# Optimization experiments

Measured on AMD Instinct MI355X. Metric: run time of the kernel, lower is better.

Reference implementation:

```python
import jax, jax.numpy as jnp
import numpy as np

B, D, H, E, L = 8192, 1024, 1024, 16, 2  # batch, input_dim, exp_hidden_dim, exp_num, exp_layers


def setup_inputs() -> dict:
    key = jax.random.key(0)
    ks = jax.random.split(key, 12)
    s_in = 1.0 / np.sqrt(D)
    s_h = 1.0 / np.sqrt(H)
    return {
        "x":   jax.random.normal(ks[0], (B, D), dtype=jnp.float32),
        # per-expert embedding layer (E experts fused on leading axis)
        "W1":  jax.random.uniform(ks[1], (E, D, H), jnp.float32, -s_in, s_in),
        "b1":  jax.random.uniform(ks[2], (E, H), jnp.float32, -s_in, s_in),
        # per-expert hidden layer (shared across the L repeated blocks, as in the torch code)
        "W2":  jax.random.uniform(ks[3], (E, H, H), jnp.float32, -s_h, s_h),
        "b2":  jax.random.uniform(ks[4], (E, H), jnp.float32, -s_h, s_h),
        # per-expert output layer H -> 1
        "Wo":  jax.random.uniform(ks[5], (E, H), jnp.float32, -s_h, s_h),
        "bo":  jax.random.uniform(ks[6], (E,), jnp.float32, -s_h, s_h),
        # two gates: D -> E, softmax
        "Wg1": jax.random.uniform(ks[7], (D, E), jnp.float32, -s_in, s_in),
        "bg1": jax.random.uniform(ks[8], (E,), jnp.float32, -s_in, s_in),
        "Wg2": jax.random.uniform(ks[9], (D, E), jnp.float32, -s_in, s_in),
        "bg2": jax.random.uniform(ks[10], (E,), jnp.float32, -s_in, s_in),
    }


def reference(x, W1, b1, W2, b2, Wo, bo, Wg1, bg1, Wg2, bg2):
    # Batched experts: h [B, E, H]
    h = jax.nn.sigmoid(jnp.einsum("bd,edh->beh", x, W1) + b1)
    for _ in range(L):  # weight-shared hidden blocks (ReLU then the SAME linear)
        h = jnp.einsum("beh,ehk->bek", jax.nn.relu(h), W2) + b2
    f = jnp.einsum("beh,eh->be", h, Wo) + bo  # expert scalar outputs [B, E]
    g1 = jax.nn.softmax(x @ Wg1 + bg1, axis=-1)  # [B, E]
    g2 = jax.nn.softmax(x @ Wg2 + bg2, axis=-1)
    out1 = jnp.einsum("be,be->b", g1, f)
    out2 = jnp.einsum("be,be->b", g2, f)
    return (out1, out2)
```

## Files before the change

### kernel.cpp

```cpp
#include <hip/hip_runtime.h>
#include <hip/hip_bf16.h>
#include <cstdint>
#include <cstddef>


using half8   = __attribute__((ext_vector_type(8))) _Float16;
using floatx4 = __attribute__((ext_vector_type(4))) float;

template<int ACT>
__global__ __launch_bounds__(256, 2)
void gemm_kernel(const _Float16* __restrict__ A, const _Float16* __restrict__ Bt,
                 const float* __restrict__ bias, _Float16* __restrict__ C,
                 size_t a_estride,
                 const float* __restrict__ Wo, float* __restrict__ f, int e0)
{
    __shared__ __align__(16) _Float16 sbuf[2][24 * 512];

    const int tid  = threadIdx.x;
    const int lane = tid & 63;
    const int w    = tid >> 6;
    const int wm   = w & 1;
    const int wn   = w >> 1;

    const int flat = blockIdx.x + (blockIdx.y << 3);
    const int xcd  = flat & 7;
    int s = flat >> 3;
    const int g = gridDim.y >> 5;
    int le, mb_base;
    if (g <= 8) {
        const int p = 8 / g;
        le = xcd / p;
        mb_base = (xcd % p) * (64 / p);
    } else {
        le = (xcd << 1) | (s >> 8);
        s &= 255;
        mb_base = 0;
    }
    const int nb = (s >> 2) & 3;
    const int mb = mb_base + (s >> 4) * 4 + (s & 3);
    const int m0 = mb * 128;
    const int n0 = nb * 256;

    const _Float16* Ae = A    + (size_t)le * a_estride;
    const _Float16* Be = Bt   + (size_t)le * (1024ull * 1024ull);
    const float*    be = bias + (size_t)le * 1024ull;
    _Float16*       Ce = C    + (size_t)le * (8192ull * 1024ull);

    const int mtb_blk = m0 >> 4;
    const int ntb_blk = n0 >> 4;

    const _Float16* gs[6];
#pragma unroll
    for (int u = 0; u < 6; ++u) {
        const int fidx = w * 6 + u;
        gs[u] = (fidx < 8)
            ? (Ae + (size_t)(mtb_blk + fidx) * (32 * 512) + lane * 8)
            : (Be + (size_t)(ntb_blk + (fidx - 8)) * (32 * 512) + lane * 8);
    }

    floatx4 acc[4][8];
#pragma unroll
    for (int i = 0; i < 4; ++i)
#pragma unroll
        for (int j = 0; j < 8; ++j) { floatx4 z = {0.f, 0.f, 0.f, 0.f}; acc[i][j] = z; }

    auto STAGE = [&](_Float16* buf) {
#pragma unroll
        for (int u = 0; u < 6; ++u) {
            __builtin_amdgcn_global_load_lds(
                (const __attribute__((address_space(1))) void*)gs[u],
                (__attribute__((address_space(3))) void*)(buf + (w * 6 + u) * 512),
                16, 0, 0);
            gs[u] += 512;
        }
    };
    auto COMPUTE = [&](const _Float16* buf) {
        half8 a[4], b[8];
#pragma unroll
        for (int i = 0; i < 4; ++i)
            a[i] = *(const half8*)(buf + (wm * 4 + i) * 512 + lane * 8);
#pragma unroll
        for (int j = 0; j < 8; ++j)
            b[j] = *(const half8*)(buf + 4096 + (wn * 8 + j) * 512 + lane * 8);
#pragma unroll
        for (int i = 0; i < 4; ++i)
#pragma unroll
            for (int j = 0; j < 8; ++j)
                acc[i][j] = __builtin_amdgcn_mfma_f32_16x16x32_f16(a[i], b[j], acc[i][j], 0, 0, 0);
    };

    STAGE(sbuf[0]);
    __syncthreads();
#pragma unroll 1
    for (int c = 0; c < 30; c += 2) {
        STAGE(sbuf[1]);
        COMPUTE(sbuf[0]);
        __syncthreads();
        STAGE(sbuf[0]);
        COMPUTE(sbuf[1]);
        __syncthreads();
    }
    STAGE(sbuf[1]);
    COMPUTE(sbuf[0]);
    __syncthreads();
    COMPUTE(sbuf[1]);

    const int q   = lane >> 4;
    const int l15 = lane & 15;
    float bj[8];
#pragma unroll
    for (int j = 0; j < 8; ++j) bj[j] = be[n0 + wn * 128 + j * 16 + l15];

    if (ACT == 2) {
        const float* we = Wo + (size_t)(e0 + le) * 1024;
        float wj[8];
#pragma unroll
        for (int j = 0; j < 8; ++j) wj[j] = we[n0 + wn * 128 + j * 16 + l15];
#pragma unroll
        for (int i = 0; i < 4; ++i) {
            const int mbase = m0 + wm * 64 + i * 16 + q * 4;
#pragma unroll
            for (int r = 0; r < 4; ++r) {
                float sacc = 0.f;
#pragma unroll
                for (int j = 0; j < 8; ++j)
                    sacc += fmaxf(acc[i][j][r] + bj[j], 0.0f) * wj[j];
#pragma unroll
                for (int m = 1; m < 16; m <<= 1) sacc += __shfl_xor(sacc, m, 64);
                if (l15 == 0) atomicAdd(&f[(size_t)(mbase + r) * 16 + (e0 + le)], sacc);
            }
        }
    } else {
        __syncthreads();
        _Float16* T = &sbuf[0][0] + w * 3072;
        const int kcg0 = (n0 + wn * 128) >> 5;
#pragma unroll
        for (int i = 0; i < 4; ++i) {
#pragma unroll
            for (int j = 0; j < 8; ++j)
#pragma unroll
                for (int r = 0; r < 4; ++r) {
                    float v = acc[i][j][r] + bj[j];
                    v = 1.0f / (1.0f + __expf(-v));
                    T[(q * 4 + r) * 136 + j * 16 + l15] = (_Float16)v;
                }
            const int mt = mtb_blk + wm * 4 + i;
#pragma unroll
            for (int kci = 0; kci < 4; ++kci) {
                half8 v8 = *(const half8*)(T + l15 * 136 + kci * 32 + q * 8);
                *(half8*)(Ce + ((size_t)mt * 32 + kcg0 + kci) * 512 + lane * 8) = v8;
            }
        }
    }
}

__global__ __launch_bounds__(256)
void castx_kernel(const float* __restrict__ x, _Float16* __restrict__ xb)
{
    __shared__ _Float16 tile[64 * 72];
    const int k0 = blockIdx.x * 64;
    const int m0 = blockIdx.y * 64;
    const int tid = threadIdx.x;
    const int col4 = (tid & 15) * 4;
    const int rb   = tid >> 4;
#pragma unroll
    for (int p = 0; p < 4; ++p) {
        const int row = rb + p * 16;
        float4 a = *(const float4*)(x + (size_t)(m0 + row) * 1024 + k0 + col4);
        _Float16* d = tile + row * 72 + col4;
        d[0] = (_Float16)a.x; d[1] = (_Float16)a.y; d[2] = (_Float16)a.z; d[3] = (_Float16)a.w;
    }
    __syncthreads();
    const int lane = tid & 63, w = tid >> 6;
    const int l15 = lane & 15, q = lane >> 4;
#pragma unroll
    for (int ff = 0; ff < 2; ++ff) {
        const int fidx = w * 2 + ff;
        const int mi = fidx >> 1, kci = fidx & 1;
        half8 v = *(const half8*)(tile + (mi * 16 + l15) * 72 + kci * 32 + q * 8);
        const size_t mt = (m0 >> 4) + mi, kc = (k0 >> 5) + kci;
        *(half8*)(xb + (mt * 32 + kc) * 512 + lane * 8) = v;
    }
}

__global__ __launch_bounds__(256)
void wtr_kernel(const float* __restrict__ W1, const float* __restrict__ W2,
                _Float16* __restrict__ W1F, _Float16* __restrict__ W2F,
                const float* __restrict__ Wo, float* __restrict__ v)
{
    __shared__ _Float16 tile[64 * 73];
    const int z = blockIdx.z;
    const float* src = (z < 16) ? (W1 + (size_t)z * 1048576ull) : (W2 + (size_t)(z - 16) * 1048576ull);
    _Float16*    dst = (z < 16) ? (W1F + (size_t)z * 1048576ull) : (W2F + (size_t)(z - 16) * 1048576ull);
    const int n0 = blockIdx.x * 64;
    const int k0 = blockIdx.y * 64;
    const int tid = threadIdx.x;
    const int lane = tid & 63, w = tid >> 6;
    const int l15 = lane & 15, q = lane >> 4;

    const int col4 = l15 * 4;
    const int rbase = w * 4 + q;
    float4 a4[4];
#pragma unroll
    for (int p = 0; p < 4; ++p) {
        const int row = rbase + p * 16;
        a4[p] = *(const float4*)(src + (size_t)(k0 + row) * 1024 + n0 + col4);
        _Float16* d = tile + row * 73 + col4;
        d[0] = (_Float16)a4[p].x; d[1] = (_Float16)a4[p].y;
        d[2] = (_Float16)a4[p].z; d[3] = (_Float16)a4[p].w;
    }

    if (z >= 16) {
        const int e = z - 16;
        const float* wo = Wo + ((size_t)e << 10) + n0;
        float* ve = v + ((size_t)e << 10) + k0;
#pragma unroll
        for (int p = 0; p < 4; ++p) {
            float s = a4[p].x * wo[col4] + a4[p].y * wo[col4 + 1]
                    + a4[p].z * wo[col4 + 2] + a4[p].w * wo[col4 + 3];
            s += __shfl_xor(s, 1, 64);
            s += __shfl_xor(s, 2, 64);
            s += __shfl_xor(s, 4, 64);
            s += __shfl_xor(s, 8, 64);
            if (l15 == 0) atomicAdd(&ve[rbase + p * 16], s);
        }
    }

    __syncthreads();
#pragma unroll
    for (int ff = 0; ff < 2; ++ff) {
        const int fidx = w * 2 + ff;
        const int nti = fidx >> 1, kci = fidx & 1;
        half8 hv;
#pragma unroll
        for (int jj = 0; jj < 8; ++jj)
            hv[jj] = tile[(kci * 32 + q * 8 + jj) * 73 + nti * 16 + l15];
        const size_t nt = (n0 >> 4) + nti, kc = (k0 >> 5) + kci;
        *(half8*)(dst + (nt * 32 + kc) * 512 + lane * 8) = hv;
    }
}

__global__ __launch_bounds__(256)
void zerof_kernel(float* __restrict__ f)
{
    const size_t i = ((size_t)blockIdx.x * 256 + threadIdx.x) * 4;
    float4 z = {0.f, 0.f, 0.f, 0.f};
    *(float4*)(f + i) = z;
}

__global__ __launch_bounds__(64)
void prep_bo2_kernel(const float* __restrict__ b2, const float* __restrict__ Wo,
                     const float* __restrict__ bo, float* __restrict__ bo2)
{
    const int e = blockIdx.x;
    const int lane = threadIdx.x;
    const float* br = b2 + ((size_t)e << 10);
    const float* wo = Wo + ((size_t)e << 10);
    float s = 0.f;
#pragma unroll
    for (int t = 0; t < 16; ++t) s += br[t * 64 + lane] * wo[t * 64 + lane];
#pragma unroll
    for (int m = 1; m < 64; m <<= 1) s += __shfl_xor(s, m, 64);
    if (lane == 0) bo2[e] = s + bo[e];
}

__global__ __launch_bounds__(256)
void final_kernel(const float* __restrict__ x,
                  const float* __restrict__ Wg1, const float* __restrict__ bg1,
                  const float* __restrict__ Wg2, const float* __restrict__ bg2,
                  const float* __restrict__ f, const float* __restrict__ bo2,
                  float* __restrict__ out)
{
    const int lane = threadIdx.x & 63;
    const int w    = threadIdx.x >> 6;
    const int b    = blockIdx.x * 8 + w * 2;
    const float* xA = x + (size_t)b * 1024;
    const float* xB = xA + 1024;
    float g1A[16], g2A[16], g1B[16], g2B[16];
#pragma unroll
    for (int e = 0; e < 16; ++e) { g1A[e] = 0.f; g2A[e] = 0.f; g1B[e] = 0.f; g2B[e] = 0.f; }
#pragma unroll 2
    for (int t = 0; t < 16; ++t) {
        const int d = t * 64 + lane;
        const float xa = xA[d];
        const float xb2 = xB[d];
        const float4* w1 = (const float4*)(Wg1 + (size_t)d * 16);
        const float4* w2 = (const float4*)(Wg2 + (size_t)d * 16);
#pragma unroll
        for (int q4 = 0; q4 < 4; ++q4) {
            const float4 c1 = w1[q4];
            const float4 c2 = w2[q4];
#pragma unroll
            for (int c = 0; c < 4; ++c) {
                const int e = q4 * 4 + c;
                const float v1 = (c == 0) ? c1.x : (c == 1) ? c1.y : (c == 2) ? c1.z : c1.w;
                const float v2 = (c == 0) ? c2.x : (c == 1) ? c2.y : (c == 2) ? c2.z : c2.w;
                g1A[e] += xa * v1; g1B[e] += xb2 * v1;
                g2A[e] += xa * v2; g2B[e] += xb2 * v2;
            }
        }
    }
#pragma unroll
    for (int e = 0; e < 16; ++e) {
#pragma unroll
        for (int m = 1; m < 64; m <<= 1) {
            g1A[e] += __shfl_xor(g1A[e], m, 64);
            g2A[e] += __shfl_xor(g2A[e], m, 64);
            g1B[e] += __shfl_xor(g1B[e], m, 64);
            g2B[e] += __shfl_xor(g2B[e], m, 64);
        }
    }
    const float* fbA = f + (size_t)b * 16;
    const float* fbB = fbA + 16;
#pragma unroll
    for (int rr = 0; rr < 2; ++rr) {
        const float* gp1 = rr ? g1B : g1A;
        const float* gp2 = rr ? g2B : g2A;
        const float* fb  = rr ? fbB : fbA;
        float a1[16], a2[16], m1 = -1e30f, m2 = -1e30f;
#pragma unroll
        for (int e = 0; e < 16; ++e) {
            a1[e] = gp1[e] + bg1[e]; m1 = fmaxf(m1, a1[e]);
            a2[e] = gp2[e] + bg2[e]; m2 = fmaxf(m2, a2[e]);
        }
        float s1 = 0.f, s2 = 0.f, o1 = 0.f, o2 = 0.f;
#pragma unroll
        for (int e = 0; e < 16; ++e) {
            a1[e] = __expf(a1[e] - m1); s1 += a1[e];
            a2[e] = __expf(a2[e] - m2); s2 += a2[e];
        }
#pragma unroll
        for (int e = 0; e < 16; ++e) {
            const float fe = fb[e] + bo2[e];
            o1 += a1[e] * fe; o2 += a2[e] * fe;
        }
        if (lane == 0) { out[b + rr] = o1 / s1; out[8192 + b + rr] = o2 / s2; }
    }
}

extern "C" void kernel_launch(void* const* d_in, const int* in_sizes, int n_in,
                              void* d_out, int out_size, void* d_ws, size_t ws_size,
                              hipStream_t stream)
{
    const float* x   = (const float*)d_in[0];
    const float* W1  = (const float*)d_in[1];
    const float* b1  = (const float*)d_in[2];
    const float* W2  = (const float*)d_in[3];
    const float* b2  = (const float*)d_in[4];
    const float* Wo  = (const float*)d_in[5];
    const float* bo  = (const float*)d_in[6];
    const float* Wg1 = (const float*)d_in[7];
    const float* bg1 = (const float*)d_in[8];
    const float* Wg2 = (const float*)d_in[9];
    const float* bg2 = (const float*)d_in[10];
    float* out = (float*)d_out;

    char* ws = (char*)d_ws;
    _Float16* xb  = (_Float16*)(ws);
    _Float16* W1F = (_Float16*)(ws + 16777216ull);
    _Float16* W2F = (_Float16*)(ws + 50331648ull);
    float*    f   = (float*)   (ws + 83886080ull);
    float*    v   = (float*)   (ws + 84410368ull);
    float*    bo2 = (float*)   (ws + 84475904ull);
    char* hbase = ws + 84475968ull;

    int g = 1;
    const int cands[4] = {16, 8, 4, 2};
    for (int ci = 0; ci < 4; ++ci) {
        const size_t need = 84475968ull + (size_t)cands[ci] * 16777216ull;
        if (need <= ws_size) { g = cands[ci]; break; }
    }
    _Float16* h0 = (_Float16*)hbase;

    zerof_kernel<<<144, 256, 0, stream>>>(f);
    castx_kernel<<<dim3(16, 128), 256, 0, stream>>>(x, xb);
    wtr_kernel<<<dim3(16, 16, 32), 256, 0, stream>>>(W1, W2, W1F, W2F, Wo, v);
    prep_bo2_kernel<<<16, 64, 0, stream>>>(b2, Wo, bo, bo2);

    for (int e0 = 0; e0 < 16; e0 += g) {
        gemm_kernel<0><<<dim3(8, 32 * g), 256, 0, stream>>>(
            xb, W1F + (size_t)e0 * 1048576ull, b1 + (size_t)e0 * 1024, h0, 0,
            nullptr, nullptr, 0);
        gemm_kernel<2><<<dim3(8, 32 * g), 256, 0, stream>>>(
            h0, W2F + (size_t)e0 * 1048576ull, b2 + (size_t)e0 * 1024, h0, 8192ull * 1024ull,
            v, f, e0);
    }
    final_kernel<<<1024, 256, 0, stream>>>(x, Wg1, bg1, Wg2, bg2, f, bo2, out);
}
```

Measured before the change: 784.3 us.

## Triple-buffer LDS tiles and prefetch next fragments into registers ahead of MFMA

The GEMM main loop moves from two LDS buffers to three rotating ones. It splits compute into a register-load step and an MFMA step, so the next tile's A/B fragments are read from LDS into a second register set while the current tile's MFMAs run. The aim is to hide LDS read latency and global-to-LDS staging behind matrix math. The cost is more LDS (three 24KB buffers per block) and about 48 extra VGPRs for the second fragment set, which could raise register pressure under the 2-blocks-per-CU launch bound.

```diff
diff --git a/kernel.cpp b/kernel.cpp
--- a/kernel.cpp
+++ b/kernel.cpp
@@ -14,7 +14,7 @@
                  size_t a_estride,
                  const float* __restrict__ Wo, float* __restrict__ f, int e0)
 {
-    __shared__ __align__(16) _Float16 sbuf[2][24 * 512];
+    __shared__ __align__(16) _Float16 sbuf[3][12288];
 
     const int tid  = threadIdx.x;
     const int lane = tid & 63;
@@ -74,14 +74,15 @@
             gs[u] += 512;
         }
     };
-    auto COMPUTE = [&](const _Float16* buf) {
-        half8 a[4], b[8];
+    auto LOADREGS = [&](half8* a, half8* b, const _Float16* buf) {
 #pragma unroll
         for (int i = 0; i < 4; ++i)
             a[i] = *(const half8*)(buf + (wm * 4 + i) * 512 + lane * 8);
 #pragma unroll
         for (int j = 0; j < 8; ++j)
             b[j] = *(const half8*)(buf + 4096 + (wn * 8 + j) * 512 + lane * 8);
+    };
+    auto MFMA32 = [&](const half8* a, const half8* b) {
 #pragma unroll
         for (int i = 0; i < 4; ++i)
 #pragma unroll
@@ -89,21 +90,31 @@
                 acc[i][j] = __builtin_amdgcn_mfma_f32_16x16x32_f16(a[i], b[j], acc[i][j], 0, 0, 0);
     };
 
-    STAGE(sbuf[0]);
+    half8 aA[4], bA[8], aB[4], bB[8];
+    _Float16* p0 = &sbuf[0][0];
+    _Float16* p1 = &sbuf[1][0];
+    _Float16* p2 = &sbuf[2][0];
+
+    STAGE(p0);
+    STAGE(p1);
     __syncthreads();
+    LOADREGS(aA, bA, p0);
+
 #pragma unroll 1
     for (int c = 0; c < 30; c += 2) {
-        STAGE(sbuf[1]);
-        COMPUTE(sbuf[0]);
+        STAGE(p2);
+        LOADREGS(aB, bB, p1);
+        MFMA32(aA, bA);
         __syncthreads();
-        STAGE(sbuf[0]);
-        COMPUTE(sbuf[1]);
+        STAGE(p0);
+        LOADREGS(aA, bA, p2);
+        MFMA32(aB, bB);
         __syncthreads();
-    }
-    STAGE(sbuf[1]);
-    COMPUTE(sbuf[0]);
-    __syncthreads();
-    COMPUTE(sbuf[1]);
+        _Float16* t = p2; p2 = p1; p1 = p0; p0 = t;
+    }
+    LOADREGS(aB, bB, p1);
+    MFMA32(aA, bA);
+    MFMA32(aB, bB);
 
     const int q   = lane >> 4;
     const int l15 = lane & 15;
```

Result: no change. 797.4 us (+1.7%).
